# Kernel optimization log

Hardware: AMD Instinct MI355X
Metric: run time of the kernel (lower is better)

The kernel has to match this reference:

```python
import jax, jax.numpy as jnp
import numpy as np

L, U, D_IN, D_OUT, B = 6, 256, 784, 10, 32768  # num_layers, units, input_dim, output_dim, batch


def setup_inputs() -> dict:
    key = jax.random.key(0)
    ks = jax.random.split(key, 7)
    s = jnp.float32(0.05)  # keras 'random_normal' initializer stddev
    return {
        "x": jax.random.normal(ks[0], (B, D_IN), jnp.float32),
        "W_in": jax.random.normal(ks[1], (D_IN, U), jnp.float32) * s,
        "b_in": jax.random.normal(ks[2], (U,), jnp.float32) * s,
        "B0": jax.random.normal(ks[3], (L, U, U), jnp.float32) * s,   # per-layer B0
        "q": jax.random.normal(ks[4], (L, U), jnp.float32) * s,       # per-layer q
        "W_out": jax.random.normal(ks[5], (U, D_OUT), jnp.float32) * s,
        "b_out": jax.random.normal(ks[6], (D_OUT,), jnp.float32) * s,
    }


def reference(x, W_in, b_in, B0, q, W_out, b_out):
    u = W_in.shape[1]
    v0 = (x @ W_in + b_in).T          # (u, B)
    v1 = jnp.tanh(v0)                  # activation of layer 0 applied once before the loop

    def step(carry, params):
        v0, v1 = carry
        B0_l, q_l = params
        z = jnp.zeros((u, u), B0_l.dtype)
        # skew-symmetric block system [[0, B0], [-B0^T, 0]]
        A = jnp.block([[z, B0_l], [-B0_l.T, z]])           # (2u, 2u)
        rhs = jnp.concatenate([v0 + q_l[:, None], v1], 0)   # (2u, B)
        sol = jnp.linalg.solve(A, rhs)
        return (sol[:u], sol[u:]), None

    (v0, v1), _ = jax.lax.scan(step, (v0, v1), (B0, q))
    return v0.T @ W_out + b_out        # (B, D_OUT)
```

## Files before the change

kernel.cpp:

```cpp
#include <hip/hip_runtime.h>
#include <math.h>

#define NU      256
#define NLAYERS 6
#define NBATCH  32768
#define NDIN    784
#define NDOUT   10
#define NUSQ    65536

typedef unsigned short u16;
typedef __attribute__((ext_vector_type(8))) short s16x8;
typedef __attribute__((ext_vector_type(4))) float f32x4;

__device__ __forceinline__ u16 f2bf(float x) {
    union { float f; unsigned u; } a; a.f = x;
    const unsigned r = a.u + 0x7fffu + ((a.u >> 16) & 1u);
    return (u16)(r >> 16);
}
__device__ __forceinline__ float bf2f(u16 h) {
    union { unsigned u; float f; } a; a.u = ((unsigned)h) << 16; return a.f;
}

__device__ __forceinline__ void gl_lds16(const u16* g, u16* l) {
    __builtin_amdgcn_global_load_lds(
        (const __attribute__((address_space(1))) void*)g,
        (__attribute__((address_space(3))) void*)l, 16, 0, 0);
}

__device__ __forceinline__ float rlf(float v, int lane) {
    return __int_as_float(__builtin_amdgcn_readlane(__float_as_int(v), lane));
}

__device__ __forceinline__ unsigned pkey(float v, int row) {
    return (__float_as_uint(fabsf(v)) & 0xFFFFFF00u) | (unsigned)row;
}

__device__ __forceinline__ unsigned dpp_umax64_lane63(unsigned key) {
    unsigned t;
    t = (unsigned)__builtin_amdgcn_update_dpp(0, (int)key, 0x111, 0xf, 0xf, false);
    key = key > t ? key : t;
    t = (unsigned)__builtin_amdgcn_update_dpp(0, (int)key, 0x112, 0xf, 0xf, false);
    key = key > t ? key : t;
    t = (unsigned)__builtin_amdgcn_update_dpp(0, (int)key, 0x114, 0xf, 0xf, false);
    key = key > t ? key : t;
    t = (unsigned)__builtin_amdgcn_update_dpp(0, (int)key, 0x118, 0xf, 0xf, false);
    key = key > t ? key : t;
    t = (unsigned)__builtin_amdgcn_update_dpp(0, (int)key, 0x142, 0xf, 0xf, false);
    key = key > t ? key : t;
    t = (unsigned)__builtin_amdgcn_update_dpp(0, (int)key, 0x143, 0xf, 0xf, false);
    key = key > t ? key : t;
    return key;
}

#define COL_CASES(BODY) \
    case 0:  BODY(0);  break; case 1:  BODY(1);  break; \
    case 2:  BODY(2);  break; case 3:  BODY(3);  break; \
    case 4:  BODY(4);  break; case 5:  BODY(5);  break; \
    case 6:  BODY(6);  break; case 7:  BODY(7);  break; \
    case 8:  BODY(8);  break; case 9:  BODY(9);  break; \
    case 10: BODY(10); break; case 11: BODY(11); break; \
    case 12: BODY(12); break; case 13: BODY(13); break; \
    case 14: BODY(14); break; case 15: BODY(15); break; \
    case 16: BODY(16); break; case 17: BODY(17); break; \
    case 18: BODY(18); break; case 19: BODY(19); break; \
    case 20: BODY(20); break; case 21: BODY(21); break; \
    case 22: BODY(22); break; case 23: BODY(23); break; \
    case 24: BODY(24); break; case 25: BODY(25); break; \
    case 26: BODY(26); break; case 27: BODY(27); break; \
    case 28: BODY(28); break; case 29: BODY(29); break; \
    case 30: BODY(30); break; case 31: BODY(31); break;

__global__ __launch_bounds__(512, 2) void fused_inv_ingemm(
    const float* __restrict__ B0, const float* __restrict__ qg,
    u16* __restrict__ wnnh, u16* __restrict__ wnnl,
    u16* __restrict__ wnth, u16* __restrict__ wntl,
    float* __restrict__ bq,
    const float* __restrict__ X, const float* __restrict__ Win,
    const float* __restrict__ bin,
    u16* __restrict__ V0h, u16* __restrict__ V0l,
    u16* __restrict__ V1h, u16* __restrict__ V1l)
{
    __shared__ __align__(16) float colv[2][256];
    __shared__ int   s_p[2];
    __shared__ float s_pv[2];
    __shared__ int   pivrow[256];
    __shared__ int   ilogrow[256];
    __shared__ float qs[256];
    __shared__ float part[8][256];
    __shared__ __align__(16) float As[16][128];
    __shared__ __align__(16) float Bs[16][128];

    const int tid = threadIdx.x;

    if (blockIdx.x < NLAYERS) {
        const int layer = blockIdx.x;
        const int ct = tid & 63;
        const int wv = tid >> 6;

        float a[32][4];
        const float* Ablk = B0 + (size_t)layer * NU * NU;
#pragma unroll
        for (int j = 0; j < 4; ++j) {
            const float* rp = Ablk + (size_t)(ct*4 + j)*NU + wv*32;
#pragma unroll
            for (int i = 0; i < 32; i += 4) {
                const float4 v = *(const float4*)(rp + i);
                a[i+0][j] = v.x; a[i+1][j] = v.y; a[i+2][j] = v.z; a[i+3][j] = v.w;
            }
        }

        int used = 0;

        for (int k = 0; k < 256; ++k) {
            const int wvk = k >> 5, ikk = k & 31, buf = k & 1;

            if (wv == wvk) {
                float c0, c1, c2, c3;
#define EXT(I) { c0 = a[I][0]; c1 = a[I][1]; c2 = a[I][2]; c3 = a[I][3]; }
                switch (ikk) { COL_CASES(EXT) }
#undef EXT
                unsigned key = (used & 1) ? 0u : pkey(c0, ct*4 + 0);
                unsigned q1  = (used & 2) ? 0u : pkey(c1, ct*4 + 1); key = key > q1 ? key : q1;
                unsigned q2  = (used & 4) ? 0u : pkey(c2, ct*4 + 2); key = key > q2 ? key : q2;
                unsigned q3  = (used & 8) ? 0u : pkey(c3, ct*4 + 3); key = key > q3 ? key : q3;
                key = dpp_umax64_lane63(key);
                const int pn = __builtin_amdgcn_readlane((int)key, 63) & 255;
                float bv;
                switch (pn & 3) {
                    case 0: bv = rlf(c0, pn >> 2); break;
                    case 1: bv = rlf(c1, pn >> 2); break;
                    case 2: bv = rlf(c2, pn >> 2); break;
                    default: bv = rlf(c3, pn >> 2); break;
                }
                float4 cw; cw.x = c0; cw.y = c1; cw.z = c2; cw.w = c3;
                *(float4*)(&colv[buf][ct*4]) = cw;
                if (ct == 0) {
                    s_p[buf] = pn;
                    s_pv[buf] = 1.0f / bv;
                    pivrow[k] = pn;
                }
            }
            __syncthreads();

            const int   p      = __builtin_amdgcn_readfirstlane(s_p[buf]);
            const float pivinv = s_pv[buf];
            const int ctp = p >> 2, jp = p & 3;

            const float4 dv = *(const float4*)(&colv[buf][ct*4]);

            float prw[32];
#define BRD(J) { _Pragma("unroll") for (int i = 0; i < 32; ++i) \
                    prw[i] = rlf(a[i][J], ctp) * pivinv; }
            switch (jp) {
                case 0: BRD(0) break; case 1: BRD(1) break;
                case 2: BRD(2) break; default: BRD(3) break;
            }
#undef BRD

            if (wv == wvk) {
#define ZCOL(I) { prw[I] = pivinv; a[I][0] = 0.0f; a[I][1] = 0.0f; a[I][2] = 0.0f; a[I][3] = 0.0f; }
                switch (ikk) { COL_CASES(ZCOL) }
#undef ZCOL
            }

            const float d0 = -dv.x, d1 = -dv.y, d2 = -dv.z, d3 = -dv.w;
#pragma unroll
            for (int i = 0; i < 32; ++i) {
                const float pw = prw[i];
                a[i][0] = fmaf(d0, pw, a[i][0]);
                a[i][1] = fmaf(d1, pw, a[i][1]);
                a[i][2] = fmaf(d2, pw, a[i][2]);
                a[i][3] = fmaf(d3, pw, a[i][3]);
            }

            const bool mine = (ct == ctp);
#define OWR(J) { _Pragma("unroll") for (int i = 0; i < 32; ++i) a[i][J] = mine ? prw[i] : a[i][J]; }
            switch (jp) {
                case 0: OWR(0) break; case 1: OWR(1) break;
                case 2: OWR(2) break; default: OWR(3) break;
            }
#undef OWR
            if (mine) used |= (1 << jp);
        }
        __syncthreads();

        if (tid < 256) { ilogrow[pivrow[tid]] = tid; qs[tid] = qg[(size_t)layer*NU + tid]; }
        __syncthreads();

        {
            float s0=0.f, s1=0.f, s2=0.f, s3=0.f;
#pragma unroll
            for (int i = 0; i < 32; ++i) {
                const float qq = qs[pivrow[wv*32 + i]];
                s0 = fmaf(a[i][0], qq, s0);
                s1 = fmaf(a[i][1], qq, s1);
                s2 = fmaf(a[i][2], qq, s2);
                s3 = fmaf(a[i][3], qq, s3);
            }
            part[wv][ct*4+0] = s0; part[wv][ct*4+1] = s1;
            part[wv][ct*4+2] = s2; part[wv][ct*4+3] = s3;
        }
        __syncthreads();
        if (tid < 256) {
            float s = 0.f;
#pragma unroll
            for (int w2 = 0; w2 < 8; ++w2) s += part[w2][tid];
            bq[(size_t)layer*NU + ilogrow[tid]] = s;
        }

        u16* nh = wnnh + (size_t)layer*NUSQ; u16* nl = wnnl + (size_t)layer*NUSQ;
        u16* th = wnth + (size_t)layer*NUSQ; u16* tl = wntl + (size_t)layer*NUSQ;
#pragma unroll
        for (int j = 0; j < 4; ++j) {
            const int r = ilogrow[ct*4 + j];
#pragma unroll
            for (int i = 0; i < 32; ++i) {
                const int c = pivrow[wv*32 + i];
                const float v = a[i][j];
                const u16 h  = f2bf(v);
                const u16 lo = f2bf(v - bf2f(h));
                th[(size_t)r*NU + c] = h;  tl[(size_t)r*NU + c] = lo;
                nh[(size_t)c*NU + r] = h;  nl[(size_t)c*NU + r] = lo;
            }
        }
        return;
    }

    if (tid >= 256) return;

    const int bid = blockIdx.x - NLAYERS;
    const int m0 = (bid & 255) * 128;
    const int n0 = (bid >> 8) * 128;
    const int t  = tid;
    const int tx = t & 15, ty = t >> 4;
    const int K = NDIN;

    float acc[8][8];
#pragma unroll
    for (int i = 0; i < 8; ++i)
#pragma unroll
        for (int j = 0; j < 8; ++j) acc[i][j] = 0.0f;

    const int am = t >> 1;
    const int ak = (t & 1) * 8;
    const int bk = t >> 4;
    const int bn = (t & 15) * 8;

    for (int k0 = 0; k0 < K; k0 += 16) {
        const float* Ap = X + (size_t)(m0 + am)*K + (k0 + ak);
        const float4 a0 = *(const float4*)(Ap);
        const float4 a1 = *(const float4*)(Ap + 4);
        As[ak+0][am] = a0.x; As[ak+1][am] = a0.y; As[ak+2][am] = a0.z; As[ak+3][am] = a0.w;
        As[ak+4][am] = a1.x; As[ak+5][am] = a1.y; As[ak+6][am] = a1.z; As[ak+7][am] = a1.w;
        const float* Bp = Win + (size_t)(k0 + bk)*NU + (n0 + bn);
        const float4 b0 = *(const float4*)(Bp);
        const float4 b1 = *(const float4*)(Bp + 4);
        *(float4*)(&Bs[bk][bn])   = b0;
        *(float4*)(&Bs[bk][bn+4]) = b1;
        __syncthreads();
#pragma unroll
        for (int kk = 0; kk < 16; ++kk) {
            float af[8], bf[8];
            *(float4*)(af)   = *(const float4*)(&As[kk][ty*8]);
            *(float4*)(af+4) = *(const float4*)(&As[kk][ty*8+4]);
            *(float4*)(bf)   = *(const float4*)(&Bs[kk][tx*8]);
            *(float4*)(bf+4) = *(const float4*)(&Bs[kk][tx*8+4]);
#pragma unroll
            for (int i = 0; i < 8; ++i)
#pragma unroll
                for (int j = 0; j < 8; ++j)
                    acc[i][j] = fmaf(af[i], bf[j], acc[i][j]);
        }
        __syncthreads();
    }

#pragma unroll
    for (int i = 0; i < 8; ++i) {
        const size_t row = m0 + ty*8 + i;
        s16x8 vh, vl, th2, tl2;
#pragma unroll
        for (int j = 0; j < 8; ++j) {
            const float v = acc[i][j] + bin[n0 + tx*8 + j];
            const u16 h  = f2bf(v);
            vh[j] = (short)h; vl[j] = (short)f2bf(v - bf2f(h));
            const float tv = tanhf(v);
            const u16 h2 = f2bf(tv);
            th2[j] = (short)h2; tl2[j] = (short)f2bf(tv - bf2f(h2));
        }
        const size_t o = row*NU + n0 + tx*8;
        *(s16x8*)&V0h[o] = vh; *(s16x8*)&V0l[o] = vl;
        *(s16x8*)&V1h[o] = th2; *(s16x8*)&V1l[o] = tl2;
    }
}

__global__ __launch_bounds__(256, 2) void gemm_mfma(
    const u16* __restrict__ Ah, const u16* __restrict__ Al,
    const u16* __restrict__ Bh, const u16* __restrict__ Bl,
    u16* __restrict__ Ch, u16* __restrict__ Cl,
    const float* __restrict__ bias, const float alpha)
{
    __shared__ __align__(16) u16 lAh[64*32], lAl[64*32];
    const int t    = threadIdx.x;
    const int lane = t & 63;
    const int w    = t >> 6;
    const int qd = lane >> 4, l15 = lane & 15;
    const int m0 = blockIdx.x * 64;

    const int srow = t >> 2;
    const int skc  = (t & 3) * 8;

    f32x4 acc[4][4];
    const f32x4 z = {0.f, 0.f, 0.f, 0.f};
#pragma unroll
    for (int i = 0; i < 4; ++i)
#pragma unroll
        for (int j = 0; j < 4; ++j) acc[i][j] = z;

    for (int k0 = 0; k0 < NU; k0 += 32) {
        {
            const size_t ga = (size_t)(m0 + srow)*NU + k0 + skc;
            const int lo = srow*32 + skc;
            gl_lds16(Ah + ga, &lAh[lo]);
            gl_lds16(Al + ga, &lAl[lo]);
        }

        s16x8 bh[4], bl[4];
#pragma unroll
        for (int nt = 0; nt < 4; ++nt) {
            const size_t gb = (size_t)(w*64 + nt*16 + l15)*NU + k0 + qd*8;
            bh[nt] = *(const s16x8*)&Bh[gb];
            bl[nt] = *(const s16x8*)&Bl[gb];
        }

        __syncthreads();

        s16x8 ah[4], al[4];
#pragma unroll
        for (int mt = 0; mt < 4; ++mt) {
            const int off = (mt*16 + l15)*32 + qd*8;
            ah[mt] = *(const s16x8*)&lAh[off];
            al[mt] = *(const s16x8*)&lAl[off];
        }

#pragma unroll
        for (int mt = 0; mt < 4; ++mt)
#pragma unroll
            for (int nt = 0; nt < 4; ++nt) {
                acc[mt][nt] = __builtin_amdgcn_mfma_f32_16x16x32_bf16(ah[mt], bh[nt], acc[mt][nt], 0, 0, 0);
                acc[mt][nt] = __builtin_amdgcn_mfma_f32_16x16x32_bf16(ah[mt], bl[nt], acc[mt][nt], 0, 0, 0);
                acc[mt][nt] = __builtin_amdgcn_mfma_f32_16x16x32_bf16(al[mt], bh[nt], acc[mt][nt], 0, 0, 0);
            }
        __syncthreads();
    }

#pragma unroll
    for (int mt = 0; mt < 4; ++mt) {
#pragma unroll
        for (int nt = 0; nt < 4; ++nt) {
            const int col = w*64 + nt*16 + l15;
            const float bb = bias ? bias[col] : 0.0f;
#pragma unroll
            for (int r = 0; r < 4; ++r) {
                const int row = m0 + mt*16 + qd*4 + r;
                const float v = alpha*acc[mt][nt][r] + bb;
                const u16 h  = f2bf(v);
                const u16 lo = f2bf(v - bf2f(h));
                const size_t o = (size_t)row*NU + col;
                Ch[o] = h; Cl[o] = lo;
            }
        }
    }
}

__global__ __launch_bounds__(256) void out_gemm(
    const u16* __restrict__ V0h, const u16* __restrict__ V0l,
    const float* __restrict__ Wout,
    const float* __restrict__ bout, float* __restrict__ out)
{
    __shared__ float Ws[NU*NDOUT];
    const int t = threadIdx.x;
    for (int i = t; i < NU*NDOUT; i += 256) Ws[i] = Wout[i];
    __syncthreads();
    const int lane = t & 63;
    const int wv = t >> 6;
    const int row = blockIdx.x*4 + wv;
    float acc[NDOUT];
#pragma unroll
    for (int j = 0; j < NDOUT; ++j) acc[j] = 0.0f;
#pragma unroll
    for (int s = 0; s < 4; ++s) {
        const int k = lane + 64*s;
        const size_t o = (size_t)row*NU + k;
        const float v = bf2f(V0h[o]) + bf2f(V0l[o]);
#pragma unroll
        for (int j = 0; j < NDOUT; ++j) acc[j] = fmaf(v, Ws[k*NDOUT + j], acc[j]);
    }
#pragma unroll
    for (int off = 32; off > 0; off >>= 1) {
#pragma unroll
        for (int j = 0; j < NDOUT; ++j) acc[j] += __shfl_down(acc[j], off);
    }
    if (lane == 0) {
#pragma unroll
        for (int j = 0; j < NDOUT; ++j) out[(size_t)row*NDOUT + j] = acc[j] + bout[j];
    }
}

extern "C" void kernel_launch(void* const* d_in, const int* in_sizes, int n_in,
                              void* d_out, int out_size, void* d_ws, size_t ws_size,
                              hipStream_t stream)
{
    const float* x    = (const float*)d_in[0];
    const float* Win  = (const float*)d_in[1];
    const float* bin  = (const float*)d_in[2];
    const float* B0   = (const float*)d_in[3];
    const float* q    = (const float*)d_in[4];
    const float* Wout = (const float*)d_in[5];
    const float* bout = (const float*)d_in[6];
    float* out = (float*)d_out;

    u16* wnnh = (u16*)d_ws;
    u16* wnnl = wnnh + (size_t)NLAYERS*NUSQ;
    u16* wnth = wnnl + (size_t)NLAYERS*NUSQ;
    u16* wntl = wnth + (size_t)NLAYERS*NUSQ;
    float* bq = (float*)(wntl + (size_t)NLAYERS*NUSQ);
    u16* pl   = (u16*)(bq + NLAYERS*NU);
    const size_t PSZ = (size_t)NBATCH*NU;
    u16* sAh = pl;           u16* sAl = sAh + PSZ;
    u16* sBh = sAl + PSZ;    u16* sBl = sBh + PSZ;
    u16* sCh = sBl + PSZ;    u16* sCl = sCh + PSZ;

    fused_inv_ingemm<<<NLAYERS + 512, 512, 0, stream>>>(
        B0, q, wnnh, wnnl, wnth, wntl, bq,
        x, Win, bin, sAh, sAl, sBh, sBl);

    const dim3 ggrid(NBATCH/64);

    u16 *v0h = sAh, *v0l = sAl, *v1h = sBh, *v1l = sBl, *frh = sCh, *frl = sCl;
    for (int l = 0; l < NLAYERS; ++l) {
        const size_t wo = (size_t)l*NUSQ;
        gemm_mfma<<<ggrid, 256, 0, stream>>>(v1h, v1l, wnnh + wo, wnnl + wo,
                                             frh, frl, nullptr, -1.0f);
        gemm_mfma<<<ggrid, 256, 0, stream>>>(v0h, v0l, wnth + wo, wntl + wo,
                                             v1h, v1l, bq + (size_t)l*NU, 1.0f);
        u16* t0 = v0h; u16* t1 = v0l;
        v0h = frh; v0l = frl; frh = t0; frl = t1;
    }
    out_gemm<<<NBATCH/4, 256, 0, stream>>>(v0h, v0l, Wout, bout, out);
}
```

Measured before the change: 926.5 us.

## Tile GEMM 128x128 with LDS-staged B, pair layer GEMMs, coalesced epilogue

Replaces the 64-row, full-N GEMM tile with 128x128 tiles on a 2D grid. Both A and B are staged into LDS through global_load_lds, and the epilogue transposes results through an LDS buffer so stores are 16-byte vectors instead of scattered 2-byte writes. The two independent GEMMs in each layer are merged into one launch using a z-dimension, with an extra scratch buffer, and the unused v1 GEMM of the last layer is skipped. The cost is more LDS use, which may limit occupancy, plus a fallback path for when workspace is too small.

```diff
diff --git a/kernel.cpp b/kernel.cpp
--- a/kernel.cpp
+++ b/kernel.cpp
@@ -11,6 +11,7 @@
 typedef unsigned short u16;
 typedef __attribute__((ext_vector_type(8))) short s16x8;
 typedef __attribute__((ext_vector_type(4))) float f32x4;
+typedef __attribute__((ext_vector_type(2))) float f32x2;
 
 __device__ __forceinline__ u16 f2bf(float x) {
     union { float f; unsigned u; } a; a.f = x;
@@ -293,83 +294,115 @@
     }
 }
 
+#define GEMM_BODY(Ah, Al, Bh, Bl, Ch, Cl, bias, alpha, MB, NB)                 \
+    const int t    = threadIdx.x;                                              \
+    const int lane = t & 63;                                                   \
+    const int w    = t >> 6;                                                   \
+    const int wr = w >> 1, wc = w & 1;                                         \
+    const int qd = lane >> 4, l15 = lane & 15;                                 \
+    const int m0 = (MB) * 128, n0 = (NB) * 128;                                \
+    const int srow = t >> 2;                                                   \
+    const int skc  = (t & 3) * 8;                                              \
+    f32x4 acc[4][4];                                                           \
+    const f32x4 z = {0.f, 0.f, 0.f, 0.f};                                      \
+    _Pragma("unroll") for (int i = 0; i < 4; ++i)                              \
+        _Pragma("unroll") for (int j = 0; j < 4; ++j) acc[i][j] = z;           \
+    for (int k0 = 0; k0 < NU; k0 += 32) {                                      \
+        _Pragma("unroll") for (int half = 0; half < 2; ++half) {               \
+            const int rr = srow + half*64;                                     \
+            const size_t ga = (size_t)(m0 + rr)*NU + k0 + skc;                 \
+            const size_t gb = (size_t)(n0 + rr)*NU + k0 + skc;                 \
+            const int lo = rr*32 + skc;                                        \
+            gl_lds16((Ah) + ga, &lAh[lo]);                                     \
+            gl_lds16((Al) + ga, &lAl[lo]);                                     \
+            gl_lds16((Bh) + gb, &lBh[lo]);                                     \
+            gl_lds16((Bl) + gb, &lBl[lo]);                                     \
+        }                                                                      \
+        __syncthreads();                                                       \
+        s16x8 ah[4], al[4], bh[4], bl[4];                                      \
+        _Pragma("unroll") for (int mt = 0; mt < 4; ++mt) {                     \
+            const int off = (wr*64 + mt*16 + l15)*32 + qd*8;                   \
+            ah[mt] = *(const s16x8*)&lAh[off];                                 \
+            al[mt] = *(const s16x8*)&lAl[off];                                 \
+        }                                                                      \
+        _Pragma("unroll") for (int nt = 0; nt < 4; ++nt) {                     \
+            const int off = (wc*64 + nt*16 + l15)*32 + qd*8;                   \
+            bh[nt] = *(const s16x8*)&lBh[off];                                 \
+            bl[nt] = *(const s16x8*)&lBl[off];                                 \
+        }                                                                      \
+        _Pragma("unroll") for (int mt = 0; mt < 4; ++mt)                       \
+            _Pragma("unroll") for (int nt = 0; nt < 4; ++nt) {                 \
+                acc[mt][nt] = __builtin_amdgcn_mfma_f32_16x16x32_bf16(ah[mt], bh[nt], acc[mt][nt], 0, 0, 0); \
+                acc[mt][nt] = __builtin_amdgcn_mfma_f32_16x16x32_bf16(ah[mt], bl[nt], acc[mt][nt], 0, 0, 0); \
+                acc[mt][nt] = __builtin_amdgcn_mfma_f32_16x16x32_bf16(al[mt], bh[nt], acc[mt][nt], 0, 0, 0); \
+            }                                                                  \
+        __syncthreads();                                                       \
+    }                                                                          \
+    float bb[4];                                                               \
+    _Pragma("unroll") for (int nt = 0; nt < 4; ++nt) {                         \
+        const int col = n0 + wc*64 + nt*16 + l15;                              \
+        bb[nt] = (bias) ? (bias)[col] : 0.0f;                                  \
+    }                                                                          \
+    float* zone = &fbuf[w*2112];                                               \
+    const int s8 = lane >> 3;                                                  \
+    const int c8 = (lane & 7) * 8;                                             \
+    _Pragma("unroll") for (int p = 0; p < 2; ++p) {                            \
+        _Pragma("unroll") for (int mt2 = 0; mt2 < 2; ++mt2) {                  \
+            const int mt = 2*p + mt2;                                          \
+            _Pragma("unroll") for (int nt = 0; nt < 4; ++nt)                   \
+                _Pragma("unroll") for (int r = 0; r < 4; ++r)                  \
+                    zone[(mt2*16 + qd*4 + r)*66 + nt*16 + l15] =               \
+                        (alpha)*acc[mt][nt][r] + bb[nt];                       \
+        }                                                                      \
+        _Pragma("unroll") for (int u = 0; u < 4; ++u) {                        \
+            const int rl = u*8 + s8;                                           \
+            const float* src = &zone[rl*66 + c8];                              \
+            float v8[8];                                                       \
+            *(f32x2*)(v8)   = *(const f32x2*)(src);                            \
+            *(f32x2*)(v8+2) = *(const f32x2*)(src+2);                          \
+            *(f32x2*)(v8+4) = *(const f32x2*)(src+4);                          \
+            *(f32x2*)(v8+6) = *(const f32x2*)(src+6);                          \
+            s16x8 vh, vl;                                                      \
+            _Pragma("unroll") for (int j = 0; j < 8; ++j) {                    \
+                const u16 h = f2bf(v8[j]);                                     \
+                vh[j] = (short)h;                                              \
+                vl[j] = (short)f2bf(v8[j] - bf2f(h));                          \
+            }                                                                  \
+            const size_t o = (size_t)(m0 + wr*64 + p*32 + rl)*NU + (n0 + wc*64 + c8); \
+            *(s16x8*)&(Ch)[o] = vh;                                            \
+            *(s16x8*)&(Cl)[o] = vl;                                            \
+        }                                                                      \
+    }
+
 __global__ __launch_bounds__(256, 2) void gemm_mfma(
     const u16* __restrict__ Ah, const u16* __restrict__ Al,
     const u16* __restrict__ Bh, const u16* __restrict__ Bl,
     u16* __restrict__ Ch, u16* __restrict__ Cl,
     const float* __restrict__ bias, const float alpha)
 {
-    __shared__ __align__(16) u16 lAh[64*32], lAl[64*32];
-    const int t    = threadIdx.x;
-    const int lane = t & 63;
-    const int w    = t >> 6;
-    const int qd = lane >> 4, l15 = lane & 15;
-    const int m0 = blockIdx.x * 64;
-
-    const int srow = t >> 2;
-    const int skc  = (t & 3) * 8;
-
-    f32x4 acc[4][4];
-    const f32x4 z = {0.f, 0.f, 0.f, 0.f};
-#pragma unroll
-    for (int i = 0; i < 4; ++i)
-#pragma unroll
-        for (int j = 0; j < 4; ++j) acc[i][j] = z;
-
-    for (int k0 = 0; k0 < NU; k0 += 32) {
-        {
-            const size_t ga = (size_t)(m0 + srow)*NU + k0 + skc;
-            const int lo = srow*32 + skc;
-            gl_lds16(Ah + ga, &lAh[lo]);
-            gl_lds16(Al + ga, &lAl[lo]);
-        }
-
-        s16x8 bh[4], bl[4];
-#pragma unroll
-        for (int nt = 0; nt < 4; ++nt) {
-            const size_t gb = (size_t)(w*64 + nt*16 + l15)*NU + k0 + qd*8;
-            bh[nt] = *(const s16x8*)&Bh[gb];
-            bl[nt] = *(const s16x8*)&Bl[gb];
-        }
-
-        __syncthreads();
-
-        s16x8 ah[4], al[4];
-#pragma unroll
-        for (int mt = 0; mt < 4; ++mt) {
-            const int off = (mt*16 + l15)*32 + qd*8;
-            ah[mt] = *(const s16x8*)&lAh[off];
-            al[mt] = *(const s16x8*)&lAl[off];
-        }
-
-#pragma unroll
-        for (int mt = 0; mt < 4; ++mt)
-#pragma unroll
-            for (int nt = 0; nt < 4; ++nt) {
-                acc[mt][nt] = __builtin_amdgcn_mfma_f32_16x16x32_bf16(ah[mt], bh[nt], acc[mt][nt], 0, 0, 0);
-                acc[mt][nt] = __builtin_amdgcn_mfma_f32_16x16x32_bf16(ah[mt], bl[nt], acc[mt][nt], 0, 0, 0);
-                acc[mt][nt] = __builtin_amdgcn_mfma_f32_16x16x32_bf16(al[mt], bh[nt], acc[mt][nt], 0, 0, 0);
-            }
-        __syncthreads();
-    }
-
-#pragma unroll
-    for (int mt = 0; mt < 4; ++mt) {
-#pragma unroll
-        for (int nt = 0; nt < 4; ++nt) {
-            const int col = w*64 + nt*16 + l15;
-            const float bb = bias ? bias[col] : 0.0f;
-#pragma unroll
-            for (int r = 0; r < 4; ++r) {
-                const int row = m0 + mt*16 + qd*4 + r;
-                const float v = alpha*acc[mt][nt][r] + bb;
-                const u16 h  = f2bf(v);
-                const u16 lo = f2bf(v - bf2f(h));
-                const size_t o = (size_t)row*NU + col;
-                Ch[o] = h; Cl[o] = lo;
-            }
-        }
-    }
+    __shared__ __align__(16) u16 lAh[128*32], lAl[128*32], lBh[128*32], lBl[128*32];
+    __shared__ __align__(16) float fbuf[4*2112];
+    GEMM_BODY(Ah, Al, Bh, Bl, Ch, Cl, bias, alpha, blockIdx.x, blockIdx.y)
+}
+
+__global__ __launch_bounds__(256, 2) void gemm_pair(
+    const u16* __restrict__ A1h, const u16* __restrict__ A1l,
+    const u16* __restrict__ B1h, const u16* __restrict__ B1l,
+    u16* __restrict__ C1h, u16* __restrict__ C1l,
+    const u16* __restrict__ A2h, const u16* __restrict__ A2l,
+    const u16* __restrict__ B2h, const u16* __restrict__ B2l,
+    u16* __restrict__ C2h, u16* __restrict__ C2l,
+    const float* __restrict__ bias2)
+{
+    __shared__ __align__(16) u16 lAh[128*32], lAl[128*32], lBh[128*32], lBl[128*32];
+    __shared__ __align__(16) float fbuf[4*2112];
+    const int pr = blockIdx.z;
+    const u16* Ah = pr ? A2h : A1h;  const u16* Al = pr ? A2l : A1l;
+    const u16* Bh = pr ? B2h : B1h;  const u16* Bl = pr ? B2l : B1l;
+    u16* Ch = pr ? C2h : C1h;        u16* Cl = pr ? C2l : C1l;
+    const float* bias = pr ? bias2 : nullptr;
+    const float alpha = pr ? 1.0f : -1.0f;
+    GEMM_BODY(Ah, Al, Bh, Bl, Ch, Cl, bias, alpha, blockIdx.x, blockIdx.y)
 }
 
 __global__ __launch_bounds__(256) void out_gemm(
@@ -426,25 +459,46 @@
     float* bq = (float*)(wntl + (size_t)NLAYERS*NUSQ);
     u16* pl   = (u16*)(bq + NLAYERS*NU);
     const size_t PSZ = (size_t)NBATCH*NU;
-    u16* sAh = pl;           u16* sAl = sAh + PSZ;
-    u16* sBh = sAl + PSZ;    u16* sBl = sBh + PSZ;
-    u16* sCh = sBl + PSZ;    u16* sCl = sCh + PSZ;
+
+    u16* sh[4]; u16* sl[4];
+    for (int s = 0; s < 4; ++s) { sh[s] = pl + (size_t)(2*s)*PSZ; sl[s] = pl + (size_t)(2*s+1)*PSZ; }
+    const size_t base_bytes = (size_t)((char*)pl - (char*)d_ws);
+    const bool has4 = ws_size >= base_bytes + 8*PSZ*sizeof(u16);
 
     fused_inv_ingemm<<<NLAYERS + 512, 512, 0, stream>>>(
         B0, q, wnnh, wnnl, wnth, wntl, bq,
-        x, Win, bin, sAh, sAl, sBh, sBl);
-
-    const dim3 ggrid(NBATCH/64);
-
-    u16 *v0h = sAh, *v0l = sAl, *v1h = sBh, *v1l = sBl, *frh = sCh, *frl = sCl;
-    for (int l = 0; l < NLAYERS; ++l) {
-        const size_t wo = (size_t)l*NUSQ;
-        gemm_mfma<<<ggrid, 256, 0, stream>>>(v1h, v1l, wnnh + wo, wnnl + wo,
-                                             frh, frl, nullptr, -1.0f);
-        gemm_mfma<<<ggrid, 256, 0, stream>>>(v0h, v0l, wnth + wo, wntl + wo,
-                                             v1h, v1l, bq + (size_t)l*NU, 1.0f);
-        u16* t0 = v0h; u16* t1 = v0l;
-        v0h = frh; v0l = frl; frh = t0; frl = t1;
-    }
-    out_gemm<<<NBATCH/4, 256, 0, stream>>>(v0h, v0l, Wout, bout, out);
-}
+        x, Win, bin, sh[0], sl[0], sh[1], sl[1]);
+
+    const dim3 ggrid(NBATCH/128, NU/128);
+    const dim3 pgrid(NBATCH/128, NU/128, 2);
+
+    if (has4) {
+        int iv0 = 0, iv1 = 1, f0 = 2, f1 = 3;
+        for (int l = 0; l < NLAYERS - 1; ++l) {
+            const size_t wo = (size_t)l*NUSQ;
+            gemm_pair<<<pgrid, 256, 0, stream>>>(
+                sh[iv1], sl[iv1], wnnh + wo, wnnl + wo, sh[f0], sl[f0],
+                sh[iv0], sl[iv0], wnth + wo, wntl + wo, sh[f1], sl[f1],
+                bq + (size_t)l*NU);
+            const int t0 = iv0, t1 = iv1;
+            iv0 = f0; iv1 = f1; f0 = t0; f1 = t1;
+        }
+        const size_t wo = (size_t)(NLAYERS - 1)*NUSQ;
+        gemm_mfma<<<ggrid, 256, 0, stream>>>(sh[iv1], sl[iv1], wnnh + wo, wnnl + wo,
+                                             sh[f0], sl[f0], nullptr, -1.0f);
+        out_gemm<<<NBATCH/4, 256, 0, stream>>>(sh[f0], sl[f0], Wout, bout, out);
+    } else {
+        u16 *v0h = sh[0], *v0l = sl[0], *v1h = sh[1], *v1l = sl[1], *frh = sh[2], *frl = sl[2];
+        for (int l = 0; l < NLAYERS; ++l) {
+            const size_t wo = (size_t)l*NUSQ;
+            gemm_mfma<<<ggrid, 256, 0, stream>>>(v1h, v1l, wnnh + wo, wnnl + wo,
+                                                 frh, frl, nullptr, -1.0f);
+            if (l < NLAYERS - 1)
+                gemm_mfma<<<ggrid, 256, 0, stream>>>(v0h, v0l, wnth + wo, wntl + wo,
+                                                     v1h, v1l, bq + (size_t)l*NU, 1.0f);
+            u16* t0 = v0h; u16* t1 = v0l;
+            v0h = frh; v0l = frl; frh = t0; frl = t1;
+        }
+        out_gemm<<<NBATCH/4, 256, 0, stream>>>(v0h, v0l, Wout, bout, out);
+    }
+}
```

Result: faster. 837.8 us (-9.6%).
